# Kernel tuning notes

Hardware: AMD Instinct MI355X
Metric: run time of the kernel (lower is better)

The kernel has to match this reference:

```python
import jax, jax.numpy as jnp
import numpy as np
import math

PATCH = 32
NBINS = 36
EPS = 1e-18
PI = math.pi


def _sobel_grads(patch):
    # kornia SpatialGradient('sobel', 1, normalized=True): cross-correlation with
    # sobel kernels divided by sum(|k|)=8, replicate padding. out: [B,2,H,W]
    kx = jnp.array([[-1., 0., 1.], [-2., 0., 2.], [-1., 0., 1.]], dtype=patch.dtype) / 8.0
    ky = kx.T
    k = jnp.stack([kx, ky])[:, None]  # [2,1,3,3] OIHW
    p = jnp.pad(patch, ((0, 0), (0, 0), (1, 1), (1, 1)), mode='edge')
    return jax.lax.conv_general_dilated(p, k, (1, 1), 'VALID',
                                        dimension_numbers=('NCHW', 'OIHW', 'NCHW'))


def setup_inputs() -> dict:
    key = jax.random.key(0)
    B = 32768
    patch = jax.random.normal(key, (B, 1, PATCH, PATCH), dtype=jnp.float32)
    # default conf: gauss_weighted=False, circular_kernel=False -> ones kernel
    weight_kernel = jnp.ones((PATCH, PATCH), dtype=jnp.float32)
    # hard-coded circular Conv1d smoothing weights
    smooth_w = jnp.array([0.33, 0.34, 0.33], dtype=jnp.float32)
    return {"patch": patch, "weight_kernel": weight_kernel, "smooth_w": smooth_w}


def reference(patch, weight_kernel, smooth_w):
    B = patch.shape[0]
    HW = PATCH * PATCH
    g = _sobel_grads(patch) * weight_kernel          # [B,2,32,32]
    gx, gy = g[:, 0], g[:, 1]
    mag = jnp.sqrt(gx * gx + gy * gy + EPS)
    ori = jnp.arctan2(gy, gx + EPS) + 2.0 * PI
    # soft binning: linear split of magnitude between two adjacent angular bins
    o_big = NBINS * (ori + PI) / (2.0 * PI)
    bo0f = jnp.floor(o_big)
    w1 = o_big - bo0f
    bo0 = jnp.mod(bo0f, NBINS).astype(jnp.int32)
    bo1 = jnp.mod(bo0 + 1, NBINS)
    wo0 = (1.0 - w1) * mag
    wo1 = w1 * mag
    # fused scatter-histogram (replaces the 36-iteration mask+avg_pool loop);
    # adaptive_avg_pool2d(...,(1,1)) == mean over HW == scatter-sum / HW
    base = (jnp.arange(B, dtype=jnp.int32) * NBINS)[:, None]   # [B,1]
    ids = jnp.concatenate([(base + bo0.reshape(B, HW)).reshape(-1),
                           (base + bo1.reshape(B, HW)).reshape(-1)])
    vals = jnp.concatenate([wo0.reshape(-1), wo1.reshape(-1)])
    hist = jax.ops.segment_sum(vals, ids, num_segments=B * NBINS).reshape(B, NBINS) / HW
    # circular conv1d, kernel size 3, padding 1: out[i] = w0*h[i-1] + w1*h[i] + w2*h[i+1]
    hist_s = (smooth_w[0] * jnp.roll(hist, 1, axis=1)
              + smooth_w[1] * hist
              + smooth_w[2] * jnp.roll(hist, -1, axis=1))
    values = jnp.max(hist_s, axis=1)                 # [B]
    indices = jnp.argmax(hist_s, axis=1)             # [B]
    ip1 = jnp.mod(indices + 1, NBINS)
    im1 = jnp.mod(indices - 1, NBINS)
    vp1 = jnp.take_along_axis(hist_s, ip1[:, None], axis=1)[:, 0]
    vm1 = jnp.take_along_axis(hist_s, im1[:, None], axis=1)[:, 0]
    # parabolic sub-bin refinement (conf['ref']=False branch)
    refinement = (vp1 - vm1) / 2.0 / (2.0 * values - (vp1 + vm1))
    idx_ref = indices.astype(patch.dtype) + refinement
    angle = -(2.0 * PI * idx_ref / float(NBINS) - PI)  # conf['refined']=True
    return angle
```

## Files before the change

kernel.cpp:

```cpp
#include <hip/hip_runtime.h>
#include <math.h>

#define PATCH   32
#define NBINS   36
#define WPB     4
#define HW_N    (PATCH*PATCH)
#define TR      34
#define TC      34
#define NREP    2


__global__ __launch_bounds__(256, 7) void patch_dom_orient_kernel(
    const float* __restrict__ patch,
    const float* __restrict__ wk,
    const float* __restrict__ sw,
    float* __restrict__ out,
    int num_patches)
{
    __shared__ float  tile[WPB][TR][TC];
    __shared__ double hist[WPB][NREP][NBINS];
    __shared__ double hsm [WPB][NBINS];
    __shared__ double ctab[37];
    __shared__ double stab[37];

    const int tid  = threadIdx.x;
    const int w    = tid >> 6;
    const int lane = tid & 63;
    const int p    = blockIdx.x * WPB + w;
    const int pc   = (p < num_patches) ? p : (num_patches - 1);

    {
        double* hf = &hist[w][0][0];
        hf[lane] = 0.0;
        if (lane < 8) hf[64 + lane] = 0.0;
    }
    if (tid < 37) {
        double a = ((double)tid - 18.0) * 0.17453292519943295;
        ctab[tid] = cos(a);
        stab[tid] = sin(a);
    }
    const float4* pp4 = reinterpret_cast<const float4*>(patch + (size_t)pc * HW_N);
    #pragma unroll
    for (int i = 0; i < 4; ++i) {
        int idx4 = i * 64 + lane;
        float4 v = pp4[idx4];
        int flat = idx4 * 4;
        int row = flat >> 5;
        int col = flat & 31;
        float* dst = &tile[w][row + 1][col + 1];
        dst[0] = v.x; dst[1] = v.y; dst[2] = v.z; dst[3] = v.w;
    }
    {
        int r = (lane >> 1) + 1;
        if (lane & 1) tile[w][r][33] = tile[w][r][32];
        else          tile[w][r][0]  = tile[w][r][1];
    }
    if (lane < 34) tile[w][0][lane]  = tile[w][1][lane];
    if (lane < 34) tile[w][33][lane] = tile[w][32][lane];
    __syncthreads();

    const float* tbase = &tile[w][0][0];
    #pragma unroll 2
    for (int i = 0; i < HW_N / 64; ++i) {
        int idx = i * 64 + lane;
        const float* c0 = tbase + idx + ((idx >> 5) << 1);

        double pmm = (double)c0[0],      pm0 = (double)c0[1],          pmp = (double)c0[2];
        double p0m = (double)c0[TC],                                   p0p = (double)c0[TC + 2];
        double ppm = (double)c0[2 * TC], pp0 = (double)c0[2 * TC + 1], ppp = (double)c0[2 * TC + 2];
        double wf  = (double)wk[idx] * 0.125;

        double d1 = pmp - pmm, d2 = p0p - p0m, d3 = ppp - ppm;
        double gx = (fma(d2, 2.0, d1) + d3) * wf;
        double e1 = ppm - pmm, e2 = pp0 - pm0, e3 = ppp - pmp;
        double gy = (fma(e2, 2.0, e1) + e3) * wf;

        double xs = gx + 1e-18;
        double m2 = fma(gx, gx, fma(gy, gy, 1e-18));

        double r0 = (double)__builtin_amdgcn_rsqf((float)m2);
        double r  = r0 * fma(-(m2 * 0.5), r0 * r0, 1.5);
        double mag = m2 * r;

        float xf = (float)xs, yf = (float)gy;
        float ax = fabsf(xf), ay = fabsf(yf);
        float mn = fminf(ax, ay), mx = fmaxf(ax, ay);
        float rr = mn * __builtin_amdgcn_rcpf(mx);
        float s2 = rr * rr;
        float at = rr * fmaf(s2, fmaf(s2, 0.0792f, -0.2885f), 0.9954f);
        if (ay > ax)   at = 1.5707963f - at;
        if (xf < 0.0f) at = 3.1415927f - at;
        at = copysignf(at, yf);
        int n = (int)rintf(at * 5.7295780f);
        n = (n < -18) ? -18 : ((n > 18) ? 18 : n);

        double cn = ctab[n + 18];
        double sn = stab[n + 18];
        double yr = fma(gy, cn, -(xs * sn));
        double z  = yr * r;
        double u  = z * z;
        double dl = z * fma(u, fma(u, fma(u, fma(u, 35.0 / 1152.0, 5.0 / 112.0),
                                          3.0 / 40.0), 1.0 / 6.0), 1.0);
        double ph2 = fma(dl, 5.729577951308232, (double)(n + 54));
        int bh = (int)ph2;
        double w1 = ph2 - floor(ph2);
        int b0 = bh - ((bh >= 36) ? 36 : 0);
        b0 = (b0 < 0) ? 0 : ((b0 > 35) ? 35 : b0);
        int b1 = (b0 == 35) ? 0 : b0 + 1;

        double wo1 = w1 * mag;
        double wo0 = mag - wo1;
        double* hrep = &hist[w][lane & (NREP - 1)][0];
        atomicAdd(&hrep[b0], wo0);
        atomicAdd(&hrep[b1], wo1);
    }
    __syncthreads();

    double hs_val = -INFINITY;
    if (lane < NBINS) {
        int im1 = (lane == 0) ? NBINS - 1 : lane - 1;
        int ip1 = (lane == NBINS - 1) ? 0 : lane + 1;
        double hm = hist[w][0][im1]  + hist[w][1][im1];
        double h0 = hist[w][0][lane] + hist[w][1][lane];
        double hp = hist[w][0][ip1]  + hist[w][1][ip1];
        hs_val = ((double)sw[0] * hm + (double)sw[1] * h0 + (double)sw[2] * hp)
                 * (1.0 / 1024.0);
        hsm[w][lane] = hs_val;
    }
    __syncthreads();

    double v  = hs_val;
    int    bi = (lane < NBINS) ? lane : 64;
    #pragma unroll
    for (int sft = 32; sft > 0; sft >>= 1) {
        double ov = __shfl_xor(v, sft, 64);
        int    oi = __shfl_xor(bi, sft, 64);
        if (ov > v || (ov == v && oi < bi)) { v = ov; bi = oi; }
    }

    if (lane == 0 && p < num_patches) {
        int ip = (bi == NBINS - 1) ? 0 : bi + 1;
        int im = (bi == 0) ? NBINS - 1 : bi - 1;
        double vp1 = hsm[w][ip];
        double vm1 = hsm[w][im];
        double refinement = ((vp1 - vm1) / 2.0) / (2.0 * v - (vp1 + vm1));
        double idx_ref = (double)bi + refinement;
        double angle = -((2.0 * M_PI * idx_ref) / 36.0 - M_PI);
        out[p] = (float)angle;
    }
}

extern "C" void kernel_launch(void* const* d_in, const int* in_sizes, int n_in,
                              void* d_out, int out_size, void* d_ws, size_t ws_size,
                              hipStream_t stream) {
    const float* patch = (const float*)d_in[0];
    const float* wk    = (const float*)d_in[1];
    const float* sw    = (const float*)d_in[2];
    float* out = (float*)d_out;

    int num_patches = in_sizes[0] / HW_N;
    int blocks = (num_patches + WPB - 1) / WPB;

    patch_dom_orient_kernel<<<blocks, 256, 0, stream>>>(patch, wk, sw, out, num_patches);
}
```

Before: 254.0 us.

## Use separable sliding-window Sobel with per-column row reuse in gradient loop

Each lane now owns one column over 16 consecutive rows instead of a flat pixel stride. It computes separable horizontal sums and differences once per row and rotates them through registers, so each row needs three shared-memory loads instead of eight neighbour loads per pixel. The bin wrap logic is also simplified by using the truncated value in place of floor and dropping the clamp. This cuts LDS traffic and float-to-double conversions, but serialises more work per lane along rows and may change the histogram atomic contention pattern.

Result: faster. 248.0 us (-2.4%).

```diff
diff --git a/kernel.cpp b/kernel.cpp
--- a/kernel.cpp
+++ b/kernel.cpp
@@ -59,60 +59,74 @@
     if (lane < 34) tile[w][33][lane] = tile[w][32][lane];
     __syncthreads();
 
-    const float* tbase = &tile[w][0][0];
-    #pragma unroll 2
-    for (int i = 0; i < HW_N / 64; ++i) {
-        int idx = i * 64 + lane;
-        const float* c0 = tbase + idx + ((idx >> 5) << 1);
+    {
+        const int c  = lane & 31;
+        const int h  = lane >> 5;
+        const int r0 = h * 16;
+        const float* rowp = &tile[w][r0][c];
+        const float* wkp  = wk + r0 * 32 + c;
+        double* hrep = &hist[w][lane & (NREP - 1)][0];
 
-        double pmm = (double)c0[0],      pm0 = (double)c0[1],          pmp = (double)c0[2];
-        double p0m = (double)c0[TC],                                   p0p = (double)c0[TC + 2];
-        double ppm = (double)c0[2 * TC], pp0 = (double)c0[2 * TC + 1], ppp = (double)c0[2 * TC + 2];
-        double wf  = (double)wk[idx] * 0.125;
+        double a0 = (double)rowp[0], b0v = (double)rowp[1], c0v = (double)rowp[2];
+        double Tm = fma(b0v, 2.0, a0) + c0v;
+        double Dm = c0v - a0;
+        rowp += TC;
+        double a1 = (double)rowp[0], b1v = (double)rowp[1], c1v = (double)rowp[2];
+        double T0 = fma(b1v, 2.0, a1) + c1v;
+        double D0 = c1v - a1;
 
-        double d1 = pmp - pmm, d2 = p0p - p0m, d3 = ppp - ppm;
-        double gx = (fma(d2, 2.0, d1) + d3) * wf;
-        double e1 = ppm - pmm, e2 = pp0 - pm0, e3 = ppp - pmp;
-        double gy = (fma(e2, 2.0, e1) + e3) * wf;
+        #pragma unroll 4
+        for (int k = 0; k < 16; ++k) {
+            rowp += TC;
+            double ar = (double)rowp[0], br = (double)rowp[1], cr = (double)rowp[2];
+            double Tp = fma(br, 2.0, ar) + cr;
+            double Dp = cr - ar;
 
-        double xs = gx + 1e-18;
-        double m2 = fma(gx, gx, fma(gy, gy, 1e-18));
+            double wf = (double)wkp[k * 32] * 0.125;
+            double gx = (fma(D0, 2.0, Dm) + Dp) * wf;
+            double gy = (Tp - Tm) * wf;
 
-        double r0 = (double)__builtin_amdgcn_rsqf((float)m2);
-        double r  = r0 * fma(-(m2 * 0.5), r0 * r0, 1.5);
-        double mag = m2 * r;
+            double xs = gx + 1e-18;
+            double m2 = fma(gx, gx, fma(gy, gy, 1e-18));
 
-        float xf = (float)xs, yf = (float)gy;
-        float ax = fabsf(xf), ay = fabsf(yf);
-        float mn = fminf(ax, ay), mx = fmaxf(ax, ay);
-        float rr = mn * __builtin_amdgcn_rcpf(mx);
-        float s2 = rr * rr;
-        float at = rr * fmaf(s2, fmaf(s2, 0.0792f, -0.2885f), 0.9954f);
-        if (ay > ax)   at = 1.5707963f - at;
-        if (xf < 0.0f) at = 3.1415927f - at;
-        at = copysignf(at, yf);
-        int n = (int)rintf(at * 5.7295780f);
-        n = (n < -18) ? -18 : ((n > 18) ? 18 : n);
+            double r0v = (double)__builtin_amdgcn_rsqf((float)m2);
+            double rr0 = r0v * fma(-(m2 * 0.5), r0v * r0v, 1.5);
+            double mag = m2 * rr0;
 
-        double cn = ctab[n + 18];
-        double sn = stab[n + 18];
-        double yr = fma(gy, cn, -(xs * sn));
-        double z  = yr * r;
-        double u  = z * z;
-        double dl = z * fma(u, fma(u, fma(u, fma(u, 35.0 / 1152.0, 5.0 / 112.0),
-                                          3.0 / 40.0), 1.0 / 6.0), 1.0);
-        double ph2 = fma(dl, 5.729577951308232, (double)(n + 54));
-        int bh = (int)ph2;
-        double w1 = ph2 - floor(ph2);
-        int b0 = bh - ((bh >= 36) ? 36 : 0);
-        b0 = (b0 < 0) ? 0 : ((b0 > 35) ? 35 : b0);
-        int b1 = (b0 == 35) ? 0 : b0 + 1;
+            float xf = (float)xs, yf = (float)gy;
+            float ax = fabsf(xf), ay = fabsf(yf);
+            float mn = fminf(ax, ay), mx = fmaxf(ax, ay);
+            float rq = mn * __builtin_amdgcn_rcpf(mx);
+            float s2 = rq * rq;
+            float at = rq * fmaf(s2, fmaf(s2, 0.0792f, -0.2885f), 0.9954f);
+            if (ay > ax)   at = 1.5707963f - at;
+            if (xf < 0.0f) at = 3.1415927f - at;
+            at = copysignf(at, yf);
+            int n = (int)rintf(at * 5.7295780f);
+            n = (n < -18) ? -18 : ((n > 18) ? 18 : n);
 
-        double wo1 = w1 * mag;
-        double wo0 = mag - wo1;
-        double* hrep = &hist[w][lane & (NREP - 1)][0];
-        atomicAdd(&hrep[b0], wo0);
-        atomicAdd(&hrep[b1], wo1);
+            double cn = ctab[n + 18];
+            double sn = stab[n + 18];
+            double yr = fma(gy, cn, -(xs * sn));
+            double z  = yr * rr0;
+            double u  = z * z;
+            double dl = z * fma(u, fma(u, fma(u, fma(u, 35.0 / 1152.0, 5.0 / 112.0),
+                                              3.0 / 40.0), 1.0 / 6.0), 1.0);
+            double ph2 = fma(dl, 5.729577951308232, (double)(n + 54));
+            int bh = (int)ph2;
+            double w1 = ph2 - (double)bh;
+            int b0 = bh;
+            if (b0 >= 36) b0 -= 36;
+            if (b0 >= 36) b0 -= 36;
+            int b1 = (b0 == 35) ? 0 : b0 + 1;
+
+            double wo1 = w1 * mag;
+            double wo0 = mag - wo1;
+            atomicAdd(&hrep[b0], wo0);
+            atomicAdd(&hrep[b1], wo1);
+
+            Tm = T0; T0 = Tp; Dm = D0; D0 = Dp;
+        }
     }
     __syncthreads();
 
```
